# Kernel tuning notes

Measured on AMD Instinct MI355X. Metric: run time of the kernel, lower is better.

The kernel has to match this reference:

```python
import jax, jax.numpy as jnp
import numpy as np

B, N, F, T, K, O = 8, 1024, 64, 32, 3, 64


def setup_inputs() -> dict:
    key = jax.random.key(0)
    k0, k1, k2, k3 = jax.random.split(key, 4)
    x = jax.random.normal(k0, (B, N, F, T), dtype=jnp.float32)
    spatial_attention = jax.random.uniform(k1, (B, N, N), dtype=jnp.float32)
    cheb = jax.random.normal(k2, (K, N, N), dtype=jnp.float32) * 0.1  # stacked T_k
    Theta = jax.random.normal(k3, (K, F, O), dtype=jnp.float32) * (1.0 / np.sqrt(F))
    return {"x": x, "spatial_attention": spatial_attention, "cheb": cheb, "Theta": Theta}


def reference(x, spatial_attention, cheb, Theta):
    # Original per-timestep, per-k loop computes:
    #   rhs[b,i,f] = sum_j (T_k[j,i] * att[b,j,i])... note: T_k_with_at.permute(0,2,1) @ x
    #   i.e. rhs[b,i,f,t] = sum_j T_k[j,i]*att[b,j,i]*x[b,j,f,t]
    # Vectorized over all timesteps t and Chebyshev orders k at once.
    rhs = jnp.einsum('kji,bji,bjft->bkift', cheb, spatial_attention, x)  # (B,K,N,F,T)
    out = jnp.einsum('bkift,kfo->biot', rhs, Theta)                      # sum over k,f
    return jax.nn.relu(out)  # (B,N,O,T)
```

## Files before the change

kernel.cpp:

```cpp
#include <hip/hip_runtime.h>
#include <stdint.h>

#define Bn 8
#define Nn 1024
#define Fn 64
#define Tn 32
#define Kn 3
#define On 64
#define Rn (Kn * Nn)
#define Cn (On * Tn)
#define NT (Rn / 64)

typedef __bf16 bf16x8 __attribute__((ext_vector_type(8)));
typedef float f32x4 __attribute__((ext_vector_type(4)));
typedef __attribute__((address_space(1))) void gvoid;
typedef __attribute__((address_space(3))) void lvoid;

union BF8 { bf16x8 v; ushort s[8]; uint4 q; };

static __device__ __forceinline__ ushort f2bf(float f) {
  uint32_t u = __float_as_uint(f);
  return (ushort)((u + 0x7FFFu + ((u >> 16) & 1u)) >> 16);
}

static __device__ __forceinline__ void glds(const ushort* g, ushort* l) {
  __builtin_amdgcn_global_load_lds((gvoid*)g, (lvoid*)l, 16, 0, 0);
}

__global__ void k_thetaT(const float* __restrict__ Theta, ushort* __restrict__ ThT) {
  int idx = blockIdx.x * 256 + threadIdx.x;
  if (idx < Kn * On * Fn) {
    int k = idx / (On * Fn);
    int rem = idx % (On * Fn);
    int o = rem / Fn, f = rem % Fn;
    ThT[idx] = f2bf(Theta[(k * Fn + f) * On + o]);
  }
}

__global__ __launch_bounds__(256) void k_prepW(const float* __restrict__ att,
                                               const float* __restrict__ cheb,
                                               ushort* __restrict__ Wt) {
  __shared__ float tile[32][33];
  int i0 = blockIdx.x * 32, j0 = blockIdx.y * 32;
  int tid = threadIdx.x;
  int ci = tid & 31, rj = tid >> 5;
  float cv[4][Kn];
#pragma unroll
  for (int p = 0; p < 4; p++) {
    int j = j0 + rj + p * 8;
#pragma unroll
    for (int k = 0; k < Kn; k++)
      cv[p][k] = cheb[((size_t)k * Nn + j) * Nn + i0 + ci];
  }
  for (int b = 0; b < Bn; b++) {
    float av[4];
#pragma unroll
    for (int p = 0; p < 4; p++) {
      int j = j0 + rj + p * 8;
      av[p] = att[((size_t)b * Nn + j) * Nn + i0 + ci];
    }
    for (int k = 0; k < Kn; k++) {
#pragma unroll
      for (int p = 0; p < 4; p++)
        tile[rj + p * 8][ci] = av[p] * cv[p][k];
      __syncthreads();
#pragma unroll
      for (int p = 0; p < 4; p++) {
        int i = i0 + rj + p * 8;
        Wt[((size_t)b * Nn + i) * Rn + (size_t)k * Nn + j0 + ci] = f2bf(tile[ci][rj + p * 8]);
      }
      __syncthreads();
    }
  }
}

__global__ __launch_bounds__(512) void k_prepY(const float* __restrict__ x,
                                               const ushort* __restrict__ ThT,
                                               ushort* __restrict__ Yt) {
  __shared__ ushort ylds[1024 * 32];
  int jt = blockIdx.x, b = blockIdx.y;
  int j0 = jt * 32;
  int tid = threadIdx.x;
  int lane = tid & 63, w = tid >> 6;
  int l15 = lane & 15, l4 = lane >> 4;

  BF8 bfr[4][2][2];
#pragma unroll
  for (int jj = 0; jj < 4; jj++) {
    const float* xp = x + ((size_t)b * Nn + (j0 + w * 4 + jj)) * (Fn * Tn);
#pragma unroll
    for (int ks = 0; ks < 2; ks++)
#pragma unroll
      for (int tf = 0; tf < 2; tf++) {
        int t = tf * 16 + l15;
        int fb = ks * 32 + l4 * 8;
#pragma unroll
        for (int e = 0; e < 8; e++)
          bfr[jj][ks][tf].s[e] = f2bf(xp[(fb + e) * Tn + t]);
      }
  }

  for (int k = 0; k < Kn; k++) {
    for (int h = 0; h < 2; h++) {
      BF8 afr[2][2];
#pragma unroll
      for (int o2 = 0; o2 < 2; o2++)
#pragma unroll
        for (int ks = 0; ks < 2; ks++) {
          int o = h * 32 + o2 * 16 + l15;
          afr[o2][ks].q = *(const uint4*)&ThT[((size_t)k * On + o) * Fn + ks * 32 + l4 * 8];
        }
#pragma unroll
      for (int jj = 0; jj < 4; jj++) {
        f32x4 acc[2][2] = {};
#pragma unroll
        for (int ks = 0; ks < 2; ks++)
#pragma unroll
          for (int o2 = 0; o2 < 2; o2++)
#pragma unroll
            for (int tf = 0; tf < 2; tf++)
              acc[o2][tf] = __builtin_amdgcn_mfma_f32_16x16x32_bf16(
                  afr[o2][ks].v, bfr[jj][ks][tf].v, acc[o2][tf], 0, 0, 0);
#pragma unroll
        for (int o2 = 0; o2 < 2; o2++)
#pragma unroll
          for (int tf = 0; tf < 2; tf++)
#pragma unroll
            for (int q = 0; q < 4; q++) {
              int cl = (o2 * 16 + l4 * 4 + q) * Tn + tf * 16 + l15;
              ylds[cl * 32 + w * 4 + jj] = f2bf(acc[o2][tf][q]);
            }
      }
      __syncthreads();
      const uint32_t* yl32 = (const uint32_t*)ylds;
      uint32_t* Yt32 = (uint32_t*)Yt;
      int e = tid & 15, rowst = tid >> 4;
      for (int pass = 0; pass < 32; pass++) {
        int cl = pass * 32 + rowst;
        size_t off = ((size_t)b * Cn + (size_t)(h * 1024 + cl)) * Rn + (size_t)k * Nn + j0;
        Yt32[off / 2 + e] = yl32[cl * 16 + e];
      }
      __syncthreads();
    }
  }
}

__global__ __launch_bounds__(512, 2) void k_gemm(const ushort* __restrict__ Wt,
                                                 const ushort* __restrict__ Yt,
                                                 float* __restrict__ out) {
  extern __shared__ __align__(16) ushort smem[];
  ushort* As = smem;
  ushort* Bs = smem + 32768;

  int g = blockIdx.x;
  int b = g & 7, slot = g >> 3;
  int i0 = (slot & 3) * 256, c0 = (slot >> 2) * 256;
  int tid = threadIdx.x, lane = tid & 63, w = tid >> 6;
  int l15 = lane & 15, l4 = lane >> 4;
  int wm = w >> 2, wn = w & 3;

  const ushort* Ab = Wt + ((size_t)b * Nn + i0) * Rn;
  const ushort* Bb = Yt + ((size_t)b * Cn + c0) * Rn;

  int srcC = (((lane & 7) ^ (lane >> 3)) * 8);
  int arow0 = w * 8 + (lane >> 3);
  int brow0 = (w >> 2) * 64 + (w & 3) * 8 + (lane >> 3);

  int aL = (wm * 64 + l15) * 64;
  int bL = (wn * 32 + l15) * 64;
  int x7 = l15 & 7;
  int colx0 = ((l4) ^ x7) * 8;
  int colx1 = ((4 + l4) ^ x7) * 8;

  f32x4 acc[8][4] = {};
  BF8 afX[4][2], afY[4][2];
  BF8 bfX[2][2], bfY[2][2];

#define MFMA_(a_, b_, c_) __builtin_amdgcn_mfma_f32_16x16x32_bf16((a_), (b_), (c_), 0, 0, 0)
#define BAR() asm volatile("s_barrier" ::: "memory")
#define PRIO1 __builtin_amdgcn_s_setprio(1)
#define PRIO0 __builtin_amdgcn_s_setprio(0)
#define VMC(n_) asm volatile("s_waitcnt vmcnt(" #n_ ")" ::: "memory")

#define STAGE_A(t_, h_) { int bo_ = ((t_) & 1) * 16384 + (h_) * 8192 + w * 512; \
    const ushort* gp_ = Ab + (size_t)(arow0 + (h_) * 64) * Rn + (t_) * 64 + srcC; \
    glds(gp_, As + bo_); \
    glds(gp_ + 128 * (size_t)Rn, As + bo_ + 4096); }
#define STAGE_B(t_, h_) { int bo_ = ((t_) & 1) * 16384 + (h_) * 8192 + w * 512; \
    const ushort* gp_ = Bb + (size_t)(brow0 + (h_) * 32) * Rn + (t_) * 64 + srcC; \
    glds(gp_, Bs + bo_); \
    glds(gp_ + 128 * (size_t)Rn, Bs + bo_ + 4096); }

#define RD_A(DST_, bo_, mh_) { _Pragma("unroll") for (int m = 0; m < 4; m++) { \
    int ba_ = (bo_) + (mh_) * 8192 + aL + m * 1024; \
    DST_[m][0].q = *(const uint4*)&As[ba_ + colx0]; \
    DST_[m][1].q = *(const uint4*)&As[ba_ + colx1]; } }
#define RD_B(DST_, bo_, nh_) { _Pragma("unroll") for (int n = 0; n < 2; n++) { \
    int bb_ = (bo_) + (nh_) * 8192 + bL + n * 1024; \
    DST_[n][0].q = *(const uint4*)&Bs[bb_ + colx0]; \
    DST_[n][1].q = *(const uint4*)&Bs[bb_ + colx1]; } }

#define MMC(AF_, BF_, MO_, NO_) { _Pragma("unroll") for (int ks = 0; ks < 2; ks++) \
    _Pragma("unroll") for (int m = 0; m < 4; m++) \
      _Pragma("unroll") for (int n = 0; n < 2; n++) \
        acc[(MO_) + m][(NO_) + n] = MFMA_(AF_[m][ks].v, BF_[n][ks].v, acc[(MO_) + m][(NO_) + n]); }

  STAGE_A(0, 0); STAGE_B(0, 0); STAGE_B(0, 1); STAGE_A(0, 1);
  STAGE_A(1, 0); STAGE_B(1, 0); STAGE_B(1, 1); STAGE_A(1, 1);
  VMC(8); BAR();
  RD_A(afX, 0, 0); RD_B(bfX, 0, 0);

#define TILE(t_, S2_, W1_, W2_, LAST_) { \
    int cur = ((t_) & 1) * 16384, nxt = cur ^ 16384; \
     \
    RD_B(bfY, cur, 1); \
    PRIO1; MMC(afX, bfX, 0, 0); PRIO0; \
     \
    VMC(W1_); BAR(); \
    RD_A(afY, cur, 1); \
    if (S2_) STAGE_A((t_) + 2, 0); \
    PRIO1; MMC(afX, bfY, 0, 2); PRIO0; \
    if (!(LAST_)) RD_A(afX, nxt, 0); \
     \
    VMC(W2_); BAR(); \
    if (S2_) { STAGE_B((t_) + 2, 0); STAGE_B((t_) + 2, 1); } \
    PRIO1; MMC(afY, bfX, 4, 0); PRIO0; \
    if (!(LAST_)) RD_B(bfX, nxt, 0); \
     \
    BAR(); \
    if (S2_) STAGE_A((t_) + 2, 1); \
    PRIO1; MMC(afY, bfY, 4, 2); PRIO0; \
  }

  for (int t = 0; t < NT - 2; ++t)
    TILE(t, 1, 6, 4, 0);
  TILE(NT - 2, 0, 6, 2, 0);
  TILE(NT - 1, 0, 0, 0, 1);

#undef TILE
#undef MMC
#undef RD_B
#undef RD_A
#undef STAGE_B
#undef STAGE_A
#undef VMC

  float* ob = out + (size_t)b * Nn * Cn;
#pragma unroll
  for (int m = 0; m < 8; m++) {
    int i = i0 + wm * 128 + m * 16 + l4 * 4;
#pragma unroll
    for (int n = 0; n < 4; n++) {
      int c = c0 + wn * 64 + n * 16 + l15;
#pragma unroll
      for (int q = 0; q < 4; q++)
        ob[(size_t)(i + q) * Cn + c] = fmaxf(acc[m][n][q], 0.0f);
    }
  }
}

extern "C" void kernel_launch(void* const* d_in, const int* in_sizes, int n_in,
                              void* d_out, int out_size, void* d_ws, size_t ws_size,
                              hipStream_t stream) {
  const float* x     = (const float*)d_in[0];
  const float* att   = (const float*)d_in[1];
  const float* cheb  = (const float*)d_in[2];
  const float* Theta = (const float*)d_in[3];
  float* out = (float*)d_out;

  char* ws = (char*)d_ws;
  ushort* ThT = (ushort*)ws;
  ushort* Wt  = (ushort*)(ws + 65536);
  ushort* Yt  = (ushort*)(ws + 65536 + 50331648ull);

  hipFuncSetAttribute((const void*)k_gemm, hipFuncAttributeMaxDynamicSharedMemorySize, 131072);

  k_thetaT<<<48, 256, 0, stream>>>(Theta, ThT);
  k_prepW<<<dim3(32, 32), 256, 0, stream>>>(att, cheb, Wt);
  k_prepY<<<dim3(32, 8), 512, 0, stream>>>(x, ThT, Yt);
  k_gemm<<<256, 512, 131072, stream>>>(Wt, Yt, out);
}
```

Before: 174.0 us.

## Restructure GEMM main loop into barrier-fenced ping-pong phases with single A fragment

Replaces the software-pipelined main loop, which prefetched next-tile fragments into double register buffers, with a four-phase schedule per tile. Each phase issues LDS reads and global-to-LDS stages, then runs an MFMA block between barriers after waiting on lgkmcnt(0). The aim is to reduce register pressure (one A fragment set instead of two) and to interleave waves more regularly across barriers. The cost is more barriers, extra LDS wait stalls and a shallower overlap of global staging, which could expose memory latency.

```diff
diff --git a/kernel.cpp b/kernel.cpp
--- a/kernel.cpp
+++ b/kernel.cpp
@@ -173,11 +173,12 @@
   int colx1 = ((4 + l4) ^ x7) * 8;
 
   f32x4 acc[8][4] = {};
-  BF8 afX[4][2], afY[4][2];
+  BF8 af[4][2];
   BF8 bfX[2][2], bfY[2][2];
 
 #define MFMA_(a_, b_, c_) __builtin_amdgcn_mfma_f32_16x16x32_bf16((a_), (b_), (c_), 0, 0, 0)
 #define BAR() asm volatile("s_barrier" ::: "memory")
+#define LGK0() asm volatile("s_waitcnt lgkmcnt(0)" ::: "memory")
 #define PRIO1 __builtin_amdgcn_s_setprio(1)
 #define PRIO0 __builtin_amdgcn_s_setprio(0)
 #define VMC(n_) asm volatile("s_waitcnt vmcnt(" #n_ ")" ::: "memory")
@@ -206,36 +207,33 @@
         acc[(MO_) + m][(NO_) + n] = MFMA_(AF_[m][ks].v, BF_[n][ks].v, acc[(MO_) + m][(NO_) + n]); }
 
   STAGE_A(0, 0); STAGE_B(0, 0); STAGE_B(0, 1); STAGE_A(0, 1);
-  STAGE_A(1, 0); STAGE_B(1, 0); STAGE_B(1, 1); STAGE_A(1, 1);
-  VMC(8); BAR();
-  RD_A(afX, 0, 0); RD_B(bfX, 0, 0);
-
-#define TILE(t_, S2_, W1_, W2_, LAST_) { \
-    int cur = ((t_) & 1) * 16384, nxt = cur ^ 16384; \
+  STAGE_A(1, 0); STAGE_B(1, 0); STAGE_B(1, 1);
+  VMC(6); BAR();
+
+#define TILE(t_, SA1_, SN2_, WTAIL_) { \
+    int cur = ((t_) & 1) * 16384; \
+     \
+    RD_A(af, cur, 0); RD_B(bfX, cur, 0); \
+    if (SA1_) STAGE_A((t_) + 1, 1); \
+    BAR(); LGK0(); PRIO1; MMC(af, bfX, 0, 0); PRIO0; BAR(); \
      \
     RD_B(bfY, cur, 1); \
-    PRIO1; MMC(afX, bfX, 0, 0); PRIO0; \
-     \
-    VMC(W1_); BAR(); \
-    RD_A(afY, cur, 1); \
-    if (S2_) STAGE_A((t_) + 2, 0); \
-    PRIO1; MMC(afX, bfY, 0, 2); PRIO0; \
-    if (!(LAST_)) RD_A(afX, nxt, 0); \
-     \
-    VMC(W2_); BAR(); \
-    if (S2_) { STAGE_B((t_) + 2, 0); STAGE_B((t_) + 2, 1); } \
-    PRIO1; MMC(afY, bfX, 4, 0); PRIO0; \
-    if (!(LAST_)) RD_B(bfX, nxt, 0); \
-     \
-    BAR(); \
-    if (S2_) STAGE_A((t_) + 2, 1); \
-    PRIO1; MMC(afY, bfY, 4, 2); PRIO0; \
-  }
-
-  for (int t = 0; t < NT - 2; ++t)
-    TILE(t, 1, 6, 4, 0);
-  TILE(NT - 2, 0, 6, 2, 0);
-  TILE(NT - 1, 0, 0, 0, 1);
+    if (SN2_) STAGE_A((t_) + 2, 0); \
+    BAR(); LGK0(); PRIO1; MMC(af, bfY, 0, 2); PRIO0; BAR(); \
+     \
+    RD_A(af, cur, 1); \
+    if (SN2_) STAGE_B((t_) + 2, 0); \
+    BAR(); LGK0(); PRIO1; MMC(af, bfX, 4, 0); PRIO0; BAR(); \
+     \
+    if (SN2_) STAGE_B((t_) + 2, 1); \
+    WTAIL_; \
+    BAR(); PRIO1; MMC(af, bfY, 4, 2); PRIO0; BAR(); \
+  }
+
+  for (int t = 0; t <= NT - 3; ++t)
+    TILE(t, 1, 1, VMC(6));
+  TILE(NT - 2, 1, 0, VMC(0));
+  TILE(NT - 1, 0, 0, (void)0);
 
 #undef TILE
 #undef MMC
@@ -243,7 +241,6 @@
 #undef RD_A
 #undef STAGE_B
 #undef STAGE_A
-#undef VMC
 
   float* ob = out + (size_t)b * Nn * Cn;
 #pragma unroll
```

Result: no change. 171.5 us (-1.4%).
